# Kernel tuning notes

Hardware: AMD Instinct MI355X
Metric: run time of the kernel (lower is better)

Reference implementation:

```python
import jax, jax.numpy as jnp
import numpy as np

EMBED_DIM = 1024
N_HEADS = 16
HEAD_DIM = EMBED_DIM // N_HEADS


def setup_inputs() -> dict:
    key = jax.random.key(0)
    ks = jax.random.split(key, 11)
    B, S = 4, 2048
    s = 0.02
    return {
        "queries": jax.random.normal(ks[0], (B, S, EMBED_DIM), dtype=jnp.float32),
        "keys": jax.random.normal(ks[1], (B, S, EMBED_DIM), dtype=jnp.float32),
        "values": jax.random.normal(ks[2], (B, S, EMBED_DIM), dtype=jnp.float32),
        "W_q": jax.random.normal(ks[3], (HEAD_DIM, HEAD_DIM), dtype=jnp.float32) * s,
        "b_q": jax.random.normal(ks[4], (HEAD_DIM,), dtype=jnp.float32) * s,
        "W_k": jax.random.normal(ks[5], (HEAD_DIM, HEAD_DIM), dtype=jnp.float32) * s,
        "b_k": jax.random.normal(ks[6], (HEAD_DIM,), dtype=jnp.float32) * s,
        "W_v": jax.random.normal(ks[7], (HEAD_DIM, HEAD_DIM), dtype=jnp.float32) * s,
        "b_v": jax.random.normal(ks[8], (HEAD_DIM,), dtype=jnp.float32) * s,
        "W_p": jax.random.normal(ks[9], (EMBED_DIM, EMBED_DIM), dtype=jnp.float32) * s,
        "b_p": jax.random.normal(ks[10], (EMBED_DIM,), dtype=jnp.float32) * s,
    }


def reference(queries, keys, values, W_q, b_q, W_k, b_k, W_v, b_v, W_p, b_p):
    B, S, _ = queries.shape
    scale = HEAD_DIM ** 0.5  # module uses head_dim ** (1/2)
    # split heads: [B, S, H, hd]
    q = queries.reshape(B, S, N_HEADS, HEAD_DIM)
    k = keys.reshape(B, S, N_HEADS, HEAD_DIM)
    v = values.reshape(B, S, N_HEADS, HEAD_DIM)
    # per-head projections (weights shared across heads); torch Linear: x @ W.T + b
    q = jnp.einsum('bshd,ed->bhse', q, W_q) + b_q
    k = jnp.einsum('bshd,ed->bhse', k, W_k) + b_k
    v = jnp.einsum('bshd,ed->bhse', v, W_v) + b_v
    # scaled dot-product attention
    scores = jnp.einsum('bhqd,bhkd->bhqk', q, k) / scale  # [B,H,S,S]
    attn = jax.nn.softmax(scores, axis=-1)
    ctx = jnp.einsum('bhqk,bhkd->bhqd', attn, v)  # [B,H,S,hd]
    # merge heads and final projection
    ctx = ctx.transpose(0, 2, 1, 3).reshape(B, S, EMBED_DIM)
    return ctx @ W_p.T + b_p
```

## Files before the change

### kernel.cpp

```cpp
#include <hip/hip_runtime.h>
#include <hip/hip_bf16.h>

#define EMBED 1024
#define NH 16
#define HD 64
#define BSZ 4
#define SSZ 2048
#define LSTR 72
#define BSTR 24
#define PSTR 72

typedef __attribute__((ext_vector_type(8))) short short8;
typedef __attribute__((ext_vector_type(4))) float float4v;
typedef __attribute__((ext_vector_type(2))) unsigned int uint2v;
typedef __attribute__((ext_vector_type(4))) unsigned int uint4v;

__device__ inline float4v mfma16(short8 a, short8 b, float4v c) {
    return __builtin_amdgcn_mfma_f32_16x16x32_bf16(a, b, c, 0, 0, 0);
}

__device__ inline float fexp2(float x) { return __builtin_amdgcn_exp2f(x); }

__device__ inline unsigned pk2(float a, float b) {
    unsigned ua = __builtin_bit_cast(unsigned, a) + 0x8000u;
    unsigned ub = __builtin_bit_cast(unsigned, b) + 0x8000u;
    return __builtin_amdgcn_perm(ub, ua, 0x07060302u);
}

__device__ inline short8 ld8_f32_bf16(const float* p) {
    float4v lo = *(const float4v*)p;
    float4v hi = *(const float4v*)(p + 4);
    uint4v u;
    u[0] = pk2(lo[0], lo[1]); u[1] = pk2(lo[2], lo[3]);
    u[2] = pk2(hi[0], hi[1]); u[3] = pk2(hi[2], hi[3]);
    return __builtin_bit_cast(short8, u);
}

__device__ inline void glds16(const short* gsrc, short* ldst) {
    __builtin_amdgcn_global_load_lds(
        (const __attribute__((address_space(1))) unsigned int*)gsrc,
        (__attribute__((address_space(3))) unsigned int*)ldst,
        16, 0, 0);
}

__global__ __launch_bounds__(256) void wp_cvt_kernel(
    const float* __restrict__ Wp, short* __restrict__ Wpb)
{
    int i = (blockIdx.x * 256 + threadIdx.x) * 4;
    float4v v = *(const float4v*)(Wp + i);
    uint2v s;
    s[0] = pk2(v[0], v[1]);
    s[1] = pk2(v[2], v[3]);
    *(uint2v*)(Wpb + i) = s;
}

__global__ __launch_bounds__(256) void qkv_kernel(
    const float* __restrict__ q_in, const float* __restrict__ k_in,
    const float* __restrict__ v_in,
    const float* __restrict__ Wq, const float* __restrict__ bq,
    const float* __restrict__ Wk, const float* __restrict__ bk,
    const float* __restrict__ Wv, const float* __restrict__ bv,
    short* __restrict__ qp, short* __restrict__ kp, short* __restrict__ vt)
{
    __shared__ __align__(16) short Wb[64 * LSTR];
    __shared__ __align__(16) short Bnc[4][64 * BSTR];

    int z = blockIdx.y;
    const float* X    = z == 0 ? q_in : (z == 1 ? k_in : v_in);
    const float* W    = z == 0 ? Wq   : (z == 1 ? Wk   : Wv);
    const float* bias = z == 0 ? bq   : (z == 1 ? bk   : bv);
    const float scale = z == 0 ? 0.125f * 1.44269504f : 1.0f;

    int tid = threadIdx.x;
    int wave = tid >> 6, lane = tid & 63, quad = lane >> 4, l16 = lane & 15;
    int rbase = blockIdx.x * 16;
    int b = rbase >> 11;
    int sbase = rbase & (SSZ - 1);

    {
        int wrow = tid >> 2, wc16 = (tid & 3) * 16;
        const float* wsrc = W + wrow * HD + wc16;
        *(short8*)&Wb[wrow * LSTR + wc16]     = ld8_f32_bf16(wsrc);
        *(short8*)&Wb[wrow * LSTR + wc16 + 8] = ld8_f32_bf16(wsrc + 8);
    }
    __syncthreads();

    short8 wf[4][2];
#pragma unroll
    for (int t = 0; t < 4; ++t)
#pragma unroll
        for (int c = 0; c < 2; ++c)
            wf[t][c] = *(const short8*)&Wb[(t * 16 + l16) * LSTR + c * 32 + quad * 8];

    const float* xrow = X + (size_t)(rbase + l16) * EMBED;

    if (z < 2) {
        short* Y = z == 0 ? qp : kp;
        float4v bv4[4];
#pragma unroll
        for (int dt = 0; dt < 4; ++dt)
            bv4[dt] = *(const float4v*)&bias[dt * 16 + quad * 4];
#pragma unroll
        for (int hh = 0; hh < 4; ++hh) {
            int h = wave * 4 + hh;
            const float* xs = xrow + h * HD + quad * 8;
            short8 xf0 = ld8_f32_bf16(xs);
            short8 xf1 = ld8_f32_bf16(xs + 32);
            float4v acc[4];
#pragma unroll
            for (int dt = 0; dt < 4; ++dt) acc[dt] = (float4v)(0.f);
#pragma unroll
            for (int dt = 0; dt < 4; ++dt) {
                acc[dt] = mfma16(wf[dt][0], xf0, acc[dt]);
                acc[dt] = mfma16(wf[dt][1], xf1, acc[dt]);
            }
            size_t ybase = ((size_t)(b * NH + h) * SSZ + sbase + l16) * HD;
#pragma unroll
            for (int dt = 0; dt < 4; ++dt) {
                float t0 = (acc[dt][0] + bv4[dt][0]) * scale;
                float t1 = (acc[dt][1] + bv4[dt][1]) * scale;
                float t2 = (acc[dt][2] + bv4[dt][2]) * scale;
                float t3 = (acc[dt][3] + bv4[dt][3]) * scale;
                uint2v p; p[0] = pk2(t0, t1); p[1] = pk2(t2, t3);
                *(uint2v*)&Y[ybase + dt * 16 + quad * 4] = p;
            }
        }
    } else {
        short* bw = &Bnc[wave][0];
        float bvs[4];
#pragma unroll
        for (int nt = 0; nt < 4; ++nt) bvs[nt] = bias[nt * 16 + l16];
#pragma unroll
        for (int hh = 0; hh < 4; ++hh) {
            int h = wave * 4 + hh;
            const float* xs = xrow + h * HD + quad * 8;
            short8 xf0 = ld8_f32_bf16(xs);
            short8 xf1 = ld8_f32_bf16(xs + 32);
            float4v acc[4];
#pragma unroll
            for (int nt = 0; nt < 4; ++nt) acc[nt] = (float4v)(0.f);
#pragma unroll
            for (int nt = 0; nt < 4; ++nt) {
                acc[nt] = mfma16(xf0, wf[nt][0], acc[nt]);
                acc[nt] = mfma16(xf1, wf[nt][1], acc[nt]);
            }
#pragma unroll
            for (int nt = 0; nt < 4; ++nt) {
                float t0 = acc[nt][0] + bvs[nt];
                float t1 = acc[nt][1] + bvs[nt];
                float t2 = acc[nt][2] + bvs[nt];
                float t3 = acc[nt][3] + bvs[nt];
                uint2v p; p[0] = pk2(t0, t1); p[1] = pk2(t2, t3);
                *(uint2v*)&bw[(nt * 16 + l16) * BSTR + quad * 4] = p;
            }
            short8 v0 = *(const short8*)&bw[lane * BSTR];
            short8 v1 = *(const short8*)&bw[lane * BSTR + 8];
            size_t o = ((size_t)(b * NH + h) * HD + lane) * SSZ + sbase;
            *(short8*)&vt[o] = v0;
            *(short8*)&vt[o + 8] = v1;
        }
    }
}

__global__ __launch_bounds__(512, 4) void attn_kernel(
    const short* __restrict__ qp, const short* __restrict__ kp,
    const short* __restrict__ vt, short* __restrict__ ctx)
{
    __shared__ __align__(16) short Kls[64 * 64];
    __shared__ __align__(16) short Vls[64 * 64];
    __shared__ __align__(16) short Pl[8 * 32 * PSTR];

    int tid = threadIdx.x;
    int wave = tid >> 6, lane = tid & 63, quad = lane >> 4, l16 = lane & 15;
    int bh = blockIdx.x;
    int b = bh >> 4, h = bh & 15;
    int qrow0 = blockIdx.y * 256 + wave * 32;

    const short* Qb = qp + (size_t)bh * SSZ * HD;
    const short* Kb = kp + (size_t)bh * SSZ * HD;
    const short* Vb = vt + (size_t)bh * HD * SSZ;

    int srow = tid >> 3;
    int g    = tid & 7;
    int gsw  = (g ^ (srow & 7)) * 8;
    const short* ksrc = Kb + srow * HD + g * 8;
    const short* vsrc = Vb + (size_t)srow * SSZ + g * 8;
    short* kdst = &Kls[srow * 64 + gsw];
    short* vdst = &Vls[srow * 64 + gsw];

    int xq = l16 & 7;
    int co[2];
    co[0] = ((0 + quad) ^ xq) * 8;
    co[1] = ((4 + quad) ^ xq) * 8;

    short8 qf[2][2];
#pragma unroll
    for (int nt = 0; nt < 2; ++nt)
#pragma unroll
        for (int c = 0; c < 2; ++c)
            qf[nt][c] = *(const short8*)&Qb[(size_t)(qrow0 + nt * 16 + l16) * HD + c * 32 + quad * 8];

    const short one = (short)0x3F80;
    short8 ones = {one, one, one, one, one, one, one, one};

    float4v oacc[4][2];
#pragma unroll
    for (int dt = 0; dt < 4; ++dt)
#pragma unroll
        for (int nt = 0; nt < 2; ++nt) oacc[dt][nt] = (float4v)(0.f);
    float4v lacc[2];
    lacc[0] = (float4v)(0.f); lacc[1] = (float4v)(0.f);

    short* Pw = Pl + wave * 32 * PSTR;

    {
        short8 kr = *(const short8*)(ksrc);
        short8 vr = *(const short8*)(vsrc);
        *(short8*)kdst = kr;
        *(short8*)vdst = vr;
    }
    __syncthreads();

    for (int kt = 0; kt < SSZ / 64; ++kt) {
        short8 krn, vrn;
        if (kt < 31) {
            krn = *(const short8*)(ksrc + (kt + 1) * 64 * HD);
            vrn = *(const short8*)(vsrc + (kt + 1) * 64);
        }
        float4v sacc[4][2];
#pragma unroll
        for (int mt = 0; mt < 4; ++mt) {
            sacc[mt][0] = (float4v)(0.f); sacc[mt][1] = (float4v)(0.f);
        }
#pragma unroll
        for (int mt = 0; mt < 4; ++mt)
#pragma unroll
            for (int c = 0; c < 2; ++c) {
                short8 kf = *(const short8*)&Kls[(mt * 16 + l16) * 64 + co[c]];
                sacc[mt][0] = mfma16(kf, qf[0][c], sacc[mt][0]);
                sacc[mt][1] = mfma16(kf, qf[1][c], sacc[mt][1]);
            }
#pragma unroll
        for (int mt = 0; mt < 4; ++mt)
#pragma unroll
            for (int nt = 0; nt < 2; ++nt) {
                float e0 = fexp2(sacc[mt][nt][0]);
                float e1 = fexp2(sacc[mt][nt][1]);
                float e2 = fexp2(sacc[mt][nt][2]);
                float e3 = fexp2(sacc[mt][nt][3]);
                uint2v p; p[0] = pk2(e0, e1); p[1] = pk2(e2, e3);
                *(uint2v*)&Pw[(nt * 16 + l16) * PSTR + mt * 16 + quad * 4] = p;
            }
        short8 pf[2][2];
#pragma unroll
        for (int nt = 0; nt < 2; ++nt)
#pragma unroll
            for (int c = 0; c < 2; ++c)
                pf[nt][c] = *(const short8*)&Pw[(nt * 16 + l16) * PSTR + c * 32 + quad * 8];
#pragma unroll
        for (int nt = 0; nt < 2; ++nt)
#pragma unroll
            for (int c = 0; c < 2; ++c)
                lacc[nt] = mfma16(ones, pf[nt][c], lacc[nt]);
#pragma unroll
        for (int dt = 0; dt < 4; ++dt)
#pragma unroll
            for (int c = 0; c < 2; ++c) {
                short8 vf = *(const short8*)&Vls[(dt * 16 + l16) * 64 + co[c]];
                oacc[dt][0] = mfma16(vf, pf[0][c], oacc[dt][0]);
                oacc[dt][1] = mfma16(vf, pf[1][c], oacc[dt][1]);
            }
        __syncthreads();
        if (kt < 31) {
            *(short8*)kdst = krn;
            *(short8*)vdst = vrn;
        }
        __syncthreads();
    }
    float rl[2];
    rl[0] = 1.0f / lacc[0][0];
    rl[1] = 1.0f / lacc[1][0];
#pragma unroll
    for (int dt = 0; dt < 4; ++dt)
#pragma unroll
        for (int nt = 0; nt < 2; ++nt) {
            uint2v p;
            p[0] = pk2(oacc[dt][nt][0] * rl[nt], oacc[dt][nt][1] * rl[nt]);
            p[1] = pk2(oacc[dt][nt][2] * rl[nt], oacc[dt][nt][3] * rl[nt]);
            size_t o = ((size_t)(b * SSZ + qrow0 + nt * 16 + l16)) * EMBED
                       + h * HD + dt * 16 + quad * 4;
            *(uint2v*)&ctx[o] = p;
        }
}

__global__ __launch_bounds__(256) void proj_kernel(
    const short* __restrict__ ctx, const short* __restrict__ Wpb,
    const float* __restrict__ bp, float* __restrict__ out)
{
    __shared__ __align__(16) short Als[128 * 64];
    __shared__ __align__(16) short Bls[128 * 64];

    int tid = threadIdx.x;
    int wave = tid >> 6, lane = tid & 63, quad = lane >> 4, l16 = lane & 15;
    int wm = wave >> 1, wn = wave & 1;
    int row0 = blockIdx.x * 128;
    int col0 = blockIdx.y * 128;

    int lrow = lane >> 3;
    int lcol = (lane & 7) * 8;
    const short* ag = ctx + (size_t)(row0 + wave * 32 + lrow) * EMBED + lcol;
    const short* bg = Wpb + (size_t)(col0 + wave * 32 + lrow) * EMBED + lcol;

    float4v acc[4][4];
#pragma unroll
    for (int mt = 0; mt < 4; ++mt)
#pragma unroll
        for (int nt = 0; nt < 4; ++nt) acc[mt][nt] = (float4v)(0.f);

    for (int kc = 0; kc < EMBED / 64; ++kc) {
#pragma unroll
        for (int i = 0; i < 4; ++i) {
            glds16(ag + (size_t)(i * 8) * EMBED + kc * 64,
                   &Als[(wave * 32 + i * 8) * 64]);
            glds16(bg + (size_t)(i * 8) * EMBED + kc * 64,
                   &Bls[(wave * 32 + i * 8) * 64]);
        }
        __syncthreads();
#pragma unroll
        for (int ks = 0; ks < 2; ++ks) {
            short8 af[4], bf[4];
#pragma unroll
            for (int mt = 0; mt < 4; ++mt)
                af[mt] = *(const short8*)&Als[(wm * 64 + mt * 16 + l16) * 64 + ks * 32 + quad * 8];
#pragma unroll
            for (int nt = 0; nt < 4; ++nt)
                bf[nt] = *(const short8*)&Bls[(wn * 64 + nt * 16 + l16) * 64 + ks * 32 + quad * 8];
#pragma unroll
            for (int mt = 0; mt < 4; ++mt)
#pragma unroll
                for (int nt = 0; nt < 4; ++nt)
                    acc[mt][nt] = mfma16(af[mt], bf[nt], acc[mt][nt]);
        }
        __syncthreads();
    }
#pragma unroll
    for (int nt = 0; nt < 4; ++nt) {
        float bias = bp[col0 + wn * 64 + nt * 16 + l16];
#pragma unroll
        for (int mt = 0; mt < 4; ++mt)
#pragma unroll
            for (int r = 0; r < 4; ++r) {
                int row = row0 + wm * 64 + mt * 16 + quad * 4 + r;
                out[(size_t)row * EMBED + col0 + wn * 64 + nt * 16 + l16] = acc[mt][nt][r] + bias;
            }
    }
}

extern "C" void kernel_launch(void* const* d_in, const int* in_sizes, int n_in,
                              void* d_out, int out_size, void* d_ws, size_t ws_size,
                              hipStream_t stream) {
    const float* q_in = (const float*)d_in[0];
    const float* k_in = (const float*)d_in[1];
    const float* v_in = (const float*)d_in[2];
    const float* Wq   = (const float*)d_in[3];
    const float* bq   = (const float*)d_in[4];
    const float* Wk   = (const float*)d_in[5];
    const float* bk   = (const float*)d_in[6];
    const float* Wv   = (const float*)d_in[7];
    const float* bv   = (const float*)d_in[8];
    const float* Wp   = (const float*)d_in[9];
    const float* bp   = (const float*)d_in[10];

    const size_t TENS = (size_t)BSZ * SSZ * EMBED;
    short* ws  = (short*)d_ws;
    short* qp  = ws;
    short* kp  = qp + TENS;
    short* vtp = kp + TENS;
    short* ctx = vtp + TENS;
    short* wpb = ctx + TENS;

    wp_cvt_kernel<<<dim3(EMBED * EMBED / 1024), 256, 0, stream>>>(Wp, wpb);
    qkv_kernel<<<dim3(BSZ * SSZ / 16, 3), 256, 0, stream>>>(
        q_in, k_in, v_in, Wq, bq, Wk, bk, Wv, bv, qp, kp, vtp);
    attn_kernel<<<dim3(BSZ * NH, SSZ / 256), 512, 0, stream>>>(qp, kp, vtp, ctx);
    proj_kernel<<<dim3(BSZ * SSZ / 128, EMBED / 128), 256, 0, stream>>>(
        ctx, wpb, bp, (float*)d_out);
}
```

Baseline: 284.8 us.

## Load K/V fragments directly from global into registers, drop LDS staging and barriers

```diff
diff --git a/kernel.cpp b/kernel.cpp
--- a/kernel.cpp
+++ b/kernel.cpp
@@ -24,6 +24,11 @@
 __device__ inline unsigned pk2(float a, float b) {
     unsigned ua = __builtin_bit_cast(unsigned, a) + 0x8000u;
     unsigned ub = __builtin_bit_cast(unsigned, b) + 0x8000u;
+    return __builtin_amdgcn_perm(ub, ua, 0x07060302u);
+}
+__device__ inline unsigned pk2t(float a, float b) {
+    unsigned ua = __builtin_bit_cast(unsigned, a);
+    unsigned ub = __builtin_bit_cast(unsigned, b);
     return __builtin_amdgcn_perm(ub, ua, 0x07060302u);
 }
 
@@ -162,37 +167,22 @@
     }
 }
 
-__global__ __launch_bounds__(512, 4) void attn_kernel(
+__global__ __launch_bounds__(256, 3) void attn_kernel(
     const short* __restrict__ qp, const short* __restrict__ kp,
     const short* __restrict__ vt, short* __restrict__ ctx)
 {
-    __shared__ __align__(16) short Kls[64 * 64];
-    __shared__ __align__(16) short Vls[64 * 64];
-    __shared__ __align__(16) short Pl[8 * 32 * PSTR];
+    __shared__ __align__(16) short Pl[4 * 32 * PSTR];
 
     int tid = threadIdx.x;
     int wave = tid >> 6, lane = tid & 63, quad = lane >> 4, l16 = lane & 15;
-    int bh = blockIdx.x;
+    int bh = blockIdx.y;
     int b = bh >> 4, h = bh & 15;
-    int qrow0 = blockIdx.y * 256 + wave * 32;
+    int qrow0 = blockIdx.x * 128 + wave * 32;
 
     const short* Qb = qp + (size_t)bh * SSZ * HD;
     const short* Kb = kp + (size_t)bh * SSZ * HD;
     const short* Vb = vt + (size_t)bh * HD * SSZ;
 
-    int srow = tid >> 3;
-    int g    = tid & 7;
-    int gsw  = (g ^ (srow & 7)) * 8;
-    const short* ksrc = Kb + srow * HD + g * 8;
-    const short* vsrc = Vb + (size_t)srow * SSZ + g * 8;
-    short* kdst = &Kls[srow * 64 + gsw];
-    short* vdst = &Vls[srow * 64 + gsw];
-
-    int xq = l16 & 7;
-    int co[2];
-    co[0] = ((0 + quad) ^ xq) * 8;
-    co[1] = ((4 + quad) ^ xq) * 8;
-
     short8 qf[2][2];
 #pragma unroll
     for (int nt = 0; nt < 2; ++nt)
@@ -213,33 +203,37 @@
 
     short* Pw = Pl + wave * 32 * PSTR;
 
-    {
-        short8 kr = *(const short8*)(ksrc);
-        short8 vr = *(const short8*)(vsrc);
-        *(short8*)kdst = kr;
-        *(short8*)vdst = vr;
-    }
-    __syncthreads();
+    int koff = l16 * HD + quad * 8;
+    int voff = l16 * SSZ + quad * 8;
+
+    short8 kf[4][2], vf[4][2];
+#pragma unroll
+    for (int mt = 0; mt < 4; ++mt)
+#pragma unroll
+        for (int c = 0; c < 2; ++c)
+            kf[mt][c] = *(const short8*)&Kb[koff + mt * 16 * HD + c * 32];
+#pragma unroll
+    for (int dt = 0; dt < 4; ++dt)
+#pragma unroll
+        for (int c = 0; c < 2; ++c)
+            vf[dt][c] = *(const short8*)&Vb[voff + dt * 16 * SSZ + c * 32];
 
     for (int kt = 0; kt < SSZ / 64; ++kt) {
-        short8 krn, vrn;
-        if (kt < 31) {
-            krn = *(const short8*)(ksrc + (kt + 1) * 64 * HD);
-            vrn = *(const short8*)(vsrc + (kt + 1) * 64);
-        }
+        int ktn = kt < 31 ? kt + 1 : 31;
         float4v sacc[4][2];
 #pragma unroll
         for (int mt = 0; mt < 4; ++mt) {
-            sacc[mt][0] = (float4v)(0.f); sacc[mt][1] = (float4v)(0.f);
+#pragma unroll
+            for (int nt = 0; nt < 2; ++nt) {
+                sacc[mt][nt] = mfma16(kf[mt][0], qf[nt][0], (float4v)(0.f));
+                sacc[mt][nt] = mfma16(kf[mt][1], qf[nt][1], sacc[mt][nt]);
+            }
         }
 #pragma unroll
         for (int mt = 0; mt < 4; ++mt)
 #pragma unroll
-            for (int c = 0; c < 2; ++c) {
-                short8 kf = *(const short8*)&Kls[(mt * 16 + l16) * 64 + co[c]];
-                sacc[mt][0] = mfma16(kf, qf[0][c], sacc[mt][0]);
-                sacc[mt][1] = mfma16(kf, qf[1][c], sacc[mt][1]);
-            }
+            for (int c = 0; c < 2; ++c)
+                kf[mt][c] = *(const short8*)&Kb[koff + ktn * 64 * HD + mt * 16 * HD + c * 32];
 #pragma unroll
         for (int mt = 0; mt < 4; ++mt)
 #pragma unroll
@@ -248,7 +242,7 @@
                 float e1 = fexp2(sacc[mt][nt][1]);
                 float e2 = fexp2(sacc[mt][nt][2]);
                 float e3 = fexp2(sacc[mt][nt][3]);
-                uint2v p; p[0] = pk2(e0, e1); p[1] = pk2(e2, e3);
+                uint2v p; p[0] = pk2t(e0, e1); p[1] = pk2t(e2, e3);
                 *(uint2v*)&Pw[(nt * 16 + l16) * PSTR + mt * 16 + quad * 4] = p;
             }
         short8 pf[2][2];
@@ -266,16 +260,14 @@
         for (int dt = 0; dt < 4; ++dt)
 #pragma unroll
             for (int c = 0; c < 2; ++c) {
-                short8 vf = *(const short8*)&Vls[(dt * 16 + l16) * 64 + co[c]];
-                oacc[dt][0] = mfma16(vf, pf[0][c], oacc[dt][0]);
-                oacc[dt][1] = mfma16(vf, pf[1][c], oacc[dt][1]);
-            }
-        __syncthreads();
-        if (kt < 31) {
-            *(short8*)kdst = krn;
-            *(short8*)vdst = vrn;
-        }
-        __syncthreads();
+                oacc[dt][0] = mfma16(vf[dt][c], pf[0][c], oacc[dt][0]);
+                oacc[dt][1] = mfma16(vf[dt][c], pf[1][c], oacc[dt][1]);
+            }
+#pragma unroll
+        for (int dt = 0; dt < 4; ++dt)
+#pragma unroll
+            for (int c = 0; c < 2; ++c)
+                vf[dt][c] = *(const short8*)&Vb[voff + dt * 16 * SSZ + ktn * 64 + c * 32];
     }
     float rl[2];
     rl[0] = 1.0f / lacc[0][0];
@@ -382,7 +374,7 @@
     wp_cvt_kernel<<<dim3(EMBED * EMBED / 1024), 256, 0, stream>>>(Wp, wpb);
     qkv_kernel<<<dim3(BSZ * SSZ / 16, 3), 256, 0, stream>>>(
         q_in, k_in, v_in, Wq, bq, Wk, bk, Wv, bv, qp, kp, vtp);
-    attn_kernel<<<dim3(BSZ * NH, SSZ / 256), 512, 0, stream>>>(qp, kp, vtp, ctx);
+    attn_kernel<<<dim3(SSZ / 128, BSZ * NH), 256, 0, stream>>>(qp, kp, vtp, ctx);
     proj_kernel<<<dim3(BSZ * SSZ / 128, EMBED / 128), 256, 0, stream>>>(
         ctx, wpb, bp, (float*)d_out);
 }
```

Measured after the change: 436.4 us. 53.2% more time.
